# Optimization experiments

Measured on AMD Instinct MI355X. Metric: run time of the kernel, lower is better.

The kernel has to match this reference:

```python
import jax, jax.numpy as jnp
import numpy as np

TEMPERATURE = 0.1
EPS = 1e-12  # matches torch F.normalize eps


def setup_inputs() -> dict:
    key = jax.random.key(0)
    k1, k2 = jax.random.split(key)
    B, T, C = 8, 1024, 512
    x = jax.random.normal(k1, (B, T, C), dtype=jnp.float32)
    quantized = jax.random.normal(k2, (B, T, C), dtype=jnp.float32)
    return {"x": x, "quantized": quantized}


def reference(x, quantized):
    B, T, C = x.shape
    xf = x.reshape(-1, C)            # (N, C)
    qf = quantized.reshape(-1, C)    # (N, C)
    xn = xf / jnp.maximum(jnp.linalg.norm(xf, axis=-1, keepdims=True), EPS)
    qn = qf / jnp.maximum(jnp.linalg.norm(qf, axis=-1, keepdims=True), EPS)
    # (N, N) similarity logits
    sim = jnp.matmul(xn, qn.T) / TEMPERATURE
    N = sim.shape[0]
    # cross-entropy with targets = arange(N): loss_i = logsumexp(sim_i) - sim_ii
    logZ = jax.nn.logsumexp(sim, axis=-1)
    diag = jnp.diagonal(sim)
    loss = jnp.mean(logZ - diag)
    predictions = jnp.argmax(sim, axis=-1)
    targets = jnp.arange(N)
    accuracy = jnp.mean((predictions == targets).astype(jnp.float32))
    return loss, accuracy
```

## Files before the change

### kernel.cpp

```cpp
#include <hip/hip_runtime.h>
#include <hip/hip_bf16.h>
#include <math.h>

#define CDIM 512
#define NROW 8192
#define BM 256
#define BN 256
#define BK 32
#define NT 16
#define NCB 32
#define BUFSZ 32768
#define TEMP_INV 10.0f

typedef unsigned short u16;
typedef u16  u16x8 __attribute__((ext_vector_type(8)));
typedef __bf16 bf16x8 __attribute__((ext_vector_type(8)));
typedef float  f32x4 __attribute__((ext_vector_type(4)));

static __device__ __forceinline__ float bf2f(u16 u) {
    return __uint_as_float(((unsigned)u) << 16);
}
static __device__ __forceinline__ u16 f2bf(float f) {
    unsigned u = __float_as_uint(f);
    return (u16)((u + 0x7FFFu + ((u >> 16) & 1u)) >> 16);
}

static __device__ __forceinline__ void gload_lds16(const u16* g, char* l) {
    __builtin_amdgcn_global_load_lds(
        (const __attribute__((address_space(1))) void*)g,
        (__attribute__((address_space(3))) void*)l, 16, 0, 0);
}

__global__ __launch_bounds__(256) void norm_split_kernel(
    const float* __restrict__ x, const float* __restrict__ q,
    u16* __restrict__ xh, u16* __restrict__ qh, int n)
{
    int wave = blockIdx.x * 4 + (threadIdx.x >> 6);
    int lane = threadIdx.x & 63;
    const float* src; u16* dh; int row;
    if (wave < n) { src = x; dh = xh; row = wave; }
    else          { src = q; dh = qh; row = wave - n; }

    const float4* p = reinterpret_cast<const float4*>(src + (size_t)row * CDIM);
    float4 a = p[lane * 2];
    float4 b = p[lane * 2 + 1];
    float v[8] = {a.x, a.y, a.z, a.w, b.x, b.y, b.z, b.w};
    float ss = 0.f;
#pragma unroll
    for (int j = 0; j < 8; ++j) ss += v[j] * v[j];
#pragma unroll
    for (int off = 32; off; off >>= 1) ss += __shfl_xor(ss, off);
    float scale = 1.0f / fmaxf(sqrtf(ss), 1e-12f);

    u16 h[8] __attribute__((aligned(16)));
#pragma unroll
    for (int j = 0; j < 8; ++j) h[j] = f2bf(v[j] * scale);
    *(u16x8*)&dh[(size_t)row * CDIM + lane * 8] = *(u16x8*)h;
}

__global__ __launch_bounds__(1024, 4) void sim_main_kernel(
    const u16* __restrict__ xh, const u16* __restrict__ qh,
    float4* __restrict__ part)
{
    extern __shared__ __align__(16) char smem[];
    const int t = threadIdx.x, lane = t & 63, wid = t >> 6;
    const int wm = wid >> 2, wn = wid & 3;

    const int orig = blockIdx.x;
    const int xcd = orig & 7, s = orig >> 3;
    const int rb = s >> 2;
    const int cb = xcd * 4 + (s & 3);
    const int row0 = rb * BM, col0 = cb * BN;

    const int schunk = (t & 3) ^ ((t >> 3) & 3);
    const u16* sa = xh + (size_t)(row0 + (t >> 2)) * CDIM + schunk * 8;
    const u16* sb = qh + (size_t)(col0 + (t >> 2)) * CDIM + schunk * 8;
    const unsigned dstw = (unsigned)wid * 1024u;

    auto stage = [&](int kt) {
        char* b = smem + (kt % 3) * BUFSZ;
        const int ko = kt * BK;
        gload_lds16(sa + ko, b + dstw);
        gload_lds16(sb + ko, b + 16384 + dstw);
    };

    const unsigned kxc = ((unsigned)((lane >> 4) ^ ((lane >> 1) & 3))) * 16u;
    const unsigned aro = ((unsigned)(wm * 64 + (lane & 15))) * 64u + kxc;
    const unsigned bro = 16384u + ((unsigned)(wn * 64 + (lane & 15))) * 64u + kxc;

    f32x4 acc[4][4];
#pragma unroll
    for (int i = 0; i < 4; ++i)
#pragma unroll
        for (int j = 0; j < 4; ++j) acc[i][j] = (f32x4){0.f, 0.f, 0.f, 0.f};

    stage(0); stage(1);
    asm volatile("s_waitcnt vmcnt(2)" ::: "memory");
    __builtin_amdgcn_s_barrier();
    asm volatile("" ::: "memory");

    for (int kt = 0; kt < NT; ++kt) {
        const char* buf = smem + (kt % 3) * BUFSZ;
        if (kt < NT - 2) stage(kt + 2);
        bf16x8 afr[4], bfr[4];
#pragma unroll
        for (int mf = 0; mf < 4; ++mf) afr[mf] = *(const bf16x8*)(buf + aro + mf * 1024u);
#pragma unroll
        for (int nf = 0; nf < 4; ++nf) bfr[nf] = *(const bf16x8*)(buf + bro + nf * 1024u);

        __builtin_amdgcn_s_setprio(1);
#pragma unroll
        for (int mf = 0; mf < 4; ++mf)
#pragma unroll
            for (int nf = 0; nf < 4; ++nf)
                acc[mf][nf] = __builtin_amdgcn_mfma_f32_16x16x32_bf16(
                    afr[mf], bfr[nf], acc[mf][nf], 0, 0, 0);
        __builtin_amdgcn_s_setprio(0);

        if (kt < NT - 2)       { asm volatile("s_waitcnt vmcnt(2)" ::: "memory"); }
        else if (kt == NT - 2) { asm volatile("s_waitcnt vmcnt(0)" ::: "memory"); }
        asm volatile("s_waitcnt lgkmcnt(0)" ::: "memory");
        __builtin_amdgcn_s_barrier();
        asm volatile("" ::: "memory");
    }

    __syncthreads();
    float* sm = (float*)smem;
    float* sl = sm + 1024;
    int*   si = (int*)(sl + 1024);
    float* sd = (float*)(si + 1024);
    const int g = lane >> 4;
#pragma unroll
    for (int mf = 0; mf < 4; ++mf) {
#pragma unroll
        for (int r = 0; r < 4; ++r) {
            const int row_loc  = wm * 64 + mf * 16 + g * 4 + r;
            const int row_glob = row0 + row_loc;
            const int ci = col0 + wn * 64 + (lane & 15);
            float vmax = acc[mf][0][r];
            int cbest = ci;
#pragma unroll
            for (int nf = 1; nf < 4; ++nf) {
                float v = acc[mf][nf][r];
                if (v > vmax) { vmax = v; cbest = ci + nf * 16; }
                if (ci + nf * 16 == row_glob) sd[row_loc] = v * TEMP_INV;
            }
            if (ci == row_glob) sd[row_loc] = acc[mf][0][r] * TEMP_INV;
#pragma unroll
            for (int m = 1; m < 16; m <<= 1) {
                float ov = __shfl_xor(vmax, m);
                int   oi = __shfl_xor(cbest, m);
                if (ov > vmax || (ov == vmax && oi < cbest)) { vmax = ov; cbest = oi; }
            }
            float ssum = 0.f;
#pragma unroll
            for (int nf = 0; nf < 4; ++nf)
                ssum += __expf((acc[mf][nf][r] - vmax) * TEMP_INV);
#pragma unroll
            for (int m = 1; m < 16; m <<= 1) ssum += __shfl_xor(ssum, m);
            if ((lane & 15) == 0) {
                sm[row_loc * 4 + wn] = vmax * TEMP_INV;
                sl[row_loc * 4 + wn] = ssum;
                si[row_loc * 4 + wn] = cbest;
            }
        }
    }
    __syncthreads();
    if (t < 256) {
        float M = sm[t * 4];
#pragma unroll
        for (int w = 1; w < 4; ++w) M = fmaxf(M, sm[t * 4 + w]);
        float L = 0.f;
#pragma unroll
        for (int w = 0; w < 4; ++w) L += sl[t * 4 + w] * __expf(sm[t * 4 + w] - M);
        float bv = -1e30f; int bi = 0;
#pragma unroll
        for (int w = 0; w < 4; ++w) {
            float v = sm[t * 4 + w];
            if (v > bv) { bv = v; bi = si[t * 4 + w]; }
        }
        part[(size_t)(row0 + t) * NCB + cb] =
            make_float4(M, L, __int_as_float(bi), sd[t]);
    }
}

__global__ __launch_bounds__(256) void merge_kernel(
    const float4* __restrict__ part,
    float* __restrict__ loss_arr, float* __restrict__ corr_arr)
{
    int i    = blockIdx.x * 4 + (threadIdx.x >> 6);
    int lane = threadIdx.x & 63;
    float4 v = part[(size_t)i * NCB + (lane & 31)];

    float M = v.x;
#pragma unroll
    for (int off = 32; off; off >>= 1) M = fmaxf(M, __shfl_xor(M, off));
    float L = (lane < 32) ? v.y * __expf(v.x - M) : 0.f;
#pragma unroll
    for (int off = 32; off; off >>= 1) L += __shfl_xor(L, off);
    float bm = v.x; int bi = __float_as_int(v.z);
#pragma unroll
    for (int off = 1; off < 32; off <<= 1) {
        float ov = __shfl_xor(bm, off);
        int   oi = __shfl_xor(bi, off);
        if (ov > bm || (ov == bm && oi < bi)) { bm = ov; bi = oi; }
    }
    float dg = __shfl(v.w, i >> 8);
    if (lane == 0) {
        loss_arr[i] = (M + logf(L)) - dg;
        corr_arr[i] = (bi == i) ? 1.0f : 0.0f;
    }
}

__global__ __launch_bounds__(256) void finalize_kernel(
    const float* __restrict__ loss_arr, const float* __restrict__ corr_arr,
    float* __restrict__ out, int n)
{
    float a = 0.f, b = 0.f;
    for (int i = threadIdx.x; i < n; i += 256) { a += loss_arr[i]; b += corr_arr[i]; }
#pragma unroll
    for (int off = 32; off; off >>= 1) { a += __shfl_xor(a, off); b += __shfl_xor(b, off); }
    __shared__ float sa[4], sb[4];
    int wid = threadIdx.x >> 6, lane = threadIdx.x & 63;
    if (lane == 0) { sa[wid] = a; sb[wid] = b; }
    __syncthreads();
    if (threadIdx.x == 0) {
        out[0] = (sa[0] + sa[1] + sa[2] + sa[3]) / n;
        out[1] = (sb[0] + sb[1] + sb[2] + sb[3]) / n;
    }
}

extern "C" void kernel_launch(void* const* d_in, const int* in_sizes, int n_in,
                              void* d_out, int out_size, void* d_ws, size_t ws_size,
                              hipStream_t stream)
{
    const float* x = (const float*)d_in[0];
    const float* q = (const float*)d_in[1];
    const int n = in_sizes[0] / CDIM;

    char* ws = (char*)d_ws;
    size_t sz_bf = (size_t)n * CDIM * sizeof(u16);
    u16* xh = (u16*)(ws);
    u16* qh = (u16*)(ws + sz_bf);
    char* p = ws + 2 * sz_bf;
    float4* part = (float4*)p; p += (size_t)n * NCB * sizeof(float4);
    float* loss_arr = (float*)p; p += (size_t)n * 4;
    float* corr_arr = (float*)p;

    norm_split_kernel<<<(2 * n) / 4, 256, 0, stream>>>(x, q, xh, qh, n);

    sim_main_kernel<<<(n / BM) * (n / BN), 1024, 3 * BUFSZ, stream>>>(xh, qh, part);

    merge_kernel<<<n / 4, 256, 0, stream>>>(part, loss_arr, corr_arr);

    finalize_kernel<<<1, 256, 0, stream>>>(loss_arr, corr_arr, (float*)d_out, n);
}
```

Before: 122.6 us.

## Switch similarity GEMM operands from bf16 to fp8 with halved LDS staging

The normalize kernel now packs the normalized rows into fp8 (via cvt_pk_fp8) instead of bf16, and the main similarity kernel uses fp8 MFMA 16x16x32 instructions. The LDS tile buffers, staging addressing and swizzle are reworked for 1-byte elements, so each stage issues one global-to-LDS load per thread and the per-stage footprint is halved. This cuts global and LDS traffic and uses faster fp8 matrix throughput. The cost is precision: fp8 logits scaled by 10 may perturb the logsumexp and argmax accuracy.

```diff
diff --git a/kernel.cpp b/kernel.cpp
--- a/kernel.cpp
+++ b/kernel.cpp
@@ -9,23 +9,14 @@
 #define BK 32
 #define NT 16
 #define NCB 32
-#define BUFSZ 32768
+#define BUFSZ 16384
 #define TEMP_INV 10.0f
 
+typedef unsigned char  u8;
 typedef unsigned short u16;
-typedef u16  u16x8 __attribute__((ext_vector_type(8)));
-typedef __bf16 bf16x8 __attribute__((ext_vector_type(8)));
-typedef float  f32x4 __attribute__((ext_vector_type(4)));
-
-static __device__ __forceinline__ float bf2f(u16 u) {
-    return __uint_as_float(((unsigned)u) << 16);
-}
-static __device__ __forceinline__ u16 f2bf(float f) {
-    unsigned u = __float_as_uint(f);
-    return (u16)((u + 0x7FFFu + ((u >> 16) & 1u)) >> 16);
-}
-
-static __device__ __forceinline__ void gload_lds16(const u16* g, char* l) {
+typedef float f32x4 __attribute__((ext_vector_type(4)));
+
+static __device__ __forceinline__ void gload_lds16(const u8* g, char* l) {
     __builtin_amdgcn_global_load_lds(
         (const __attribute__((address_space(1))) void*)g,
         (__attribute__((address_space(3))) void*)l, 16, 0, 0);
@@ -33,11 +24,11 @@
 
 __global__ __launch_bounds__(256) void norm_split_kernel(
     const float* __restrict__ x, const float* __restrict__ q,
-    u16* __restrict__ xh, u16* __restrict__ qh, int n)
+    u8* __restrict__ xh, u8* __restrict__ qh, int n)
 {
     int wave = blockIdx.x * 4 + (threadIdx.x >> 6);
     int lane = threadIdx.x & 63;
-    const float* src; u16* dh; int row;
+    const float* src; u8* dh; int row;
     if (wave < n) { src = x; dh = xh; row = wave; }
     else          { src = q; dh = qh; row = wave - n; }
 
@@ -52,14 +43,16 @@
     for (int off = 32; off; off >>= 1) ss += __shfl_xor(ss, off);
     float scale = 1.0f / fmaxf(sqrtf(ss), 1e-12f);
 
-    u16 h[8] __attribute__((aligned(16)));
-#pragma unroll
-    for (int j = 0; j < 8; ++j) h[j] = f2bf(v[j] * scale);
-    *(u16x8*)&dh[(size_t)row * CDIM + lane * 8] = *(u16x8*)h;
+    unsigned r0 = __builtin_amdgcn_cvt_pk_fp8_f32(v[0] * scale, v[1] * scale, 0, 0);
+    r0 = __builtin_amdgcn_cvt_pk_fp8_f32(v[2] * scale, v[3] * scale, r0, 1);
+    unsigned r1 = __builtin_amdgcn_cvt_pk_fp8_f32(v[4] * scale, v[5] * scale, 0, 0);
+    r1 = __builtin_amdgcn_cvt_pk_fp8_f32(v[6] * scale, v[7] * scale, r1, 1);
+    uint2 o; o.x = r0; o.y = r1;
+    *(uint2*)&dh[(size_t)row * CDIM + lane * 8] = o;
 }
 
 __global__ __launch_bounds__(1024, 4) void sim_main_kernel(
-    const u16* __restrict__ xh, const u16* __restrict__ qh,
+    const u8* __restrict__ xh, const u8* __restrict__ qh,
     float4* __restrict__ part)
 {
     extern __shared__ __align__(16) char smem[];
@@ -72,21 +65,23 @@
     const int cb = xcd * 4 + (s & 3);
     const int row0 = rb * BM, col0 = cb * BN;
 
-    const int schunk = (t & 3) ^ ((t >> 3) & 3);
-    const u16* sa = xh + (size_t)(row0 + (t >> 2)) * CDIM + schunk * 8;
-    const u16* sb = qh + (size_t)(col0 + (t >> 2)) * CDIM + schunk * 8;
-    const unsigned dstw = (unsigned)wid * 1024u;
+    const int isB = wid >> 3;
+    const int tt = t & 511;
+    const int rr = tt >> 1, cch = tt & 1;
+    const int m01s = ((rr >> 1) ^ (rr >> 2)) & 1;
+    const u8* srow = isB ? (qh + (size_t)(col0 + rr) * CDIM)
+                         : (xh + (size_t)(row0 + rr) * CDIM);
+    const u8* sptr = srow + (cch ^ m01s) * 16;
+    const unsigned dstw = (unsigned)(wid & 7) * 1024u + (unsigned)isB * 8192u;
 
     auto stage = [&](int kt) {
-        char* b = smem + (kt % 3) * BUFSZ;
-        const int ko = kt * BK;
-        gload_lds16(sa + ko, b + dstw);
-        gload_lds16(sb + ko, b + 16384 + dstw);
+        gload_lds16(sptr + kt * BK, smem + (kt % 3) * BUFSZ + dstw);
     };
 
-    const unsigned kxc = ((unsigned)((lane >> 4) ^ ((lane >> 1) & 3))) * 16u;
-    const unsigned aro = ((unsigned)(wm * 64 + (lane & 15))) * 64u + kxc;
-    const unsigned bro = 16384u + ((unsigned)(wn * 64 + (lane & 15))) * 64u + kxc;
+    const int r4 = lane & 15;
+    const unsigned slotx = ((unsigned)(lane >> 4)) ^ ((((r4 >> 1) ^ (r4 >> 2)) & 1) << 1);
+    const unsigned aro = ((unsigned)(wm * 64 + r4)) * 32u + slotx * 8u;
+    const unsigned bro = 8192u + ((unsigned)(wn * 64 + r4)) * 32u + slotx * 8u;
 
     f32x4 acc[4][4];
 #pragma unroll
@@ -95,29 +90,29 @@
         for (int j = 0; j < 4; ++j) acc[i][j] = (f32x4){0.f, 0.f, 0.f, 0.f};
 
     stage(0); stage(1);
-    asm volatile("s_waitcnt vmcnt(2)" ::: "memory");
+    asm volatile("s_waitcnt vmcnt(1)" ::: "memory");
     __builtin_amdgcn_s_barrier();
     asm volatile("" ::: "memory");
 
     for (int kt = 0; kt < NT; ++kt) {
         const char* buf = smem + (kt % 3) * BUFSZ;
         if (kt < NT - 2) stage(kt + 2);
-        bf16x8 afr[4], bfr[4];
-#pragma unroll
-        for (int mf = 0; mf < 4; ++mf) afr[mf] = *(const bf16x8*)(buf + aro + mf * 1024u);
-#pragma unroll
-        for (int nf = 0; nf < 4; ++nf) bfr[nf] = *(const bf16x8*)(buf + bro + nf * 1024u);
+        long afr[4], bfr[4];
+#pragma unroll
+        for (int mf = 0; mf < 4; ++mf) afr[mf] = *(const long*)(buf + aro + mf * 512u);
+#pragma unroll
+        for (int nf = 0; nf < 4; ++nf) bfr[nf] = *(const long*)(buf + bro + nf * 512u);
 
         __builtin_amdgcn_s_setprio(1);
 #pragma unroll
         for (int mf = 0; mf < 4; ++mf)
 #pragma unroll
             for (int nf = 0; nf < 4; ++nf)
-                acc[mf][nf] = __builtin_amdgcn_mfma_f32_16x16x32_bf16(
+                acc[mf][nf] = __builtin_amdgcn_mfma_f32_16x16x32_fp8_fp8(
                     afr[mf], bfr[nf], acc[mf][nf], 0, 0, 0);
         __builtin_amdgcn_s_setprio(0);
 
-        if (kt < NT - 2)       { asm volatile("s_waitcnt vmcnt(2)" ::: "memory"); }
+        if (kt < NT - 2)       { asm volatile("s_waitcnt vmcnt(1)" ::: "memory"); }
         else if (kt == NT - 2) { asm volatile("s_waitcnt vmcnt(0)" ::: "memory"); }
         asm volatile("s_waitcnt lgkmcnt(0)" ::: "memory");
         __builtin_amdgcn_s_barrier();
@@ -239,10 +234,10 @@
     const int n = in_sizes[0] / CDIM;
 
     char* ws = (char*)d_ws;
-    size_t sz_bf = (size_t)n * CDIM * sizeof(u16);
-    u16* xh = (u16*)(ws);
-    u16* qh = (u16*)(ws + sz_bf);
-    char* p = ws + 2 * sz_bf;
+    size_t sz_f8 = (size_t)n * CDIM;
+    u8* xh = (u8*)(ws);
+    u8* qh = (u8*)(ws + sz_f8);
+    char* p = ws + 2 * sz_f8;
     float4* part = (float4*)p; p += (size_t)n * NCB * sizeof(float4);
     float* loss_arr = (float*)p; p += (size_t)n * 4;
     float* corr_arr = (float*)p;
```

New measurement: 117.9 us. 1.04x faster.
